# Optimization experiments

Measured on AMD Instinct MI355X. Metric: run time of the kernel, lower is better.

Reference implementation:

```python
import jax, jax.numpy as jnp
import numpy as np

VOL_SHAPE = (192, 192, 192)
BATCH = 2
CHANNELS = 1


def setup_inputs() -> dict:
    key = jax.random.key(0)
    k1, k2 = jax.random.split(key)
    vol = jax.random.normal(k1, (BATCH,) + VOL_SHAPE + (CHANNELS,), dtype=jnp.float32)
    # near-identity affine (3,4) per batch element, as in rigid/affine motion correction
    eye = jnp.concatenate([jnp.eye(3, dtype=jnp.float32), jnp.zeros((3, 1), jnp.float32)], axis=1)
    affine = eye[None] + 0.02 * jax.random.normal(k2, (BATCH, 3, 4), dtype=jnp.float32)
    return {"vol": vol, "affine": affine}


def _warp(vol, affine):
    # vol: [B, D, H, W, C], affine: [B, 3, 4]
    B, D, H, W, C = vol.shape
    shape = (D, H, W)
    # --- affine_to_dense_shift (shift_center=True, ij indexing) ---
    ranges = [jnp.arange(s, dtype=jnp.float32) for s in shape]
    mesh = jnp.stack(jnp.meshgrid(*ranges, indexing='ij'), axis=-1)  # [D,H,W,3]
    center = jnp.array([(s - 1) / 2.0 for s in shape], dtype=jnp.float32)
    centered = mesh - center                                          # shifted grid
    homog = jnp.concatenate([centered, jnp.ones(shape + (1,), jnp.float32)], axis=-1)  # [D,H,W,4]
    loc_aff = jnp.einsum('bij,dhwj->bdhwi', affine, homog)            # [B,D,H,W,3]
    shift = loc_aff - centered                                        # dense warp field
    # --- SpatialTransformer: sample at grid + shift ---
    loc = mesh + shift                                                # [B,D,H,W,3]

    maxl = jnp.array([s - 1 for s in shape], dtype=jnp.float32)

    def interp_one(v, l):
        # v: [D,H,W,C], l: [D,H,W,3]; trilinear interp, clamp-to-edge (fill_value=None)
        cl = jnp.clip(l, 0.0, maxl)
        l0 = jnp.clip(jnp.floor(l), 0.0, maxl)
        l1 = jnp.clip(l0 + 1.0, 0.0, maxl)
        w_c0 = l1 - cl          # weight used with the floor corner (diff_loc1)
        w_c1 = 1.0 - w_c0       # weight used with the ceil corner  (diff_loc0)
        i0 = l0.astype(jnp.int32)
        i1 = l1.astype(jnp.int32)
        out = jnp.zeros(v.shape[:-1] + (v.shape[-1],), v.dtype)
        for c in range(8):  # 2^3 cube corners (fixed small loop)
            bits = ((c >> 2) & 1, (c >> 1) & 1, c & 1)
            idx = [(i1 if b else i0)[..., d] for d, b in enumerate(bits)]
            w = jnp.ones(l.shape[:-1], v.dtype)
            for d, b in enumerate(bits):
                w = w * (w_c1 if b else w_c0)[..., d]
            out = out + v[idx[0], idx[1], idx[2]] * w[..., None]
        return out

    return jax.vmap(interp_one)(vol, loc)


def reference(vol, affine):
    return _warp(vol, affine)
```

## Files before the change

### kernel.cpp

```cpp
#include <hip/hip_runtime.h>

#define DIM 192
#define NB 2

__global__ __launch_bounds__(DIM) void
SpatialTransformer_warp_kernel(const float* __restrict__ vol,
                               const float* __restrict__ affine,
                               float* __restrict__ out) {
    const int w = threadIdx.x;
    const int h = blockIdx.x;
    const int d = blockIdx.y;
    const int b = blockIdx.z;

    const float* __restrict__ A = affine + b * 12;
    const float a00 = A[0], a01 = A[1], a02 = A[2],  a03 = A[3];
    const float a10 = A[4], a11 = A[5], a12 = A[6],  a13 = A[7];
    const float a20 = A[8], a21 = A[9], a22 = A[10], a23 = A[11];

    const float center = (DIM - 1) * 0.5f;
    const float maxl   = (float)(DIM - 1);

    const float cd = (float)d - center;
    const float ch = (float)h - center;
    const float cw = (float)w - center;

    const float ld = a00 * cd + a01 * ch + a02 * cw + a03 + center;
    const float lh = a10 * cd + a11 * ch + a12 * cw + a13 + center;
    const float lw = a20 * cd + a21 * ch + a22 * cw + a23 + center;

    float cl, l0f, l1f;

    cl  = fminf(fmaxf(ld, 0.0f), maxl);
    l0f = fminf(fmaxf(floorf(ld), 0.0f), maxl);
    l1f = fminf(l0f + 1.0f, maxl);
    const float w0d = l1f - cl, w1d = 1.0f - w0d;
    const int i0d = (int)l0f, i1d = (int)l1f;

    cl  = fminf(fmaxf(lh, 0.0f), maxl);
    l0f = fminf(fmaxf(floorf(lh), 0.0f), maxl);
    l1f = fminf(l0f + 1.0f, maxl);
    const float w0h = l1f - cl, w1h = 1.0f - w0h;
    const int i0h = (int)l0f, i1h = (int)l1f;

    cl  = fminf(fmaxf(lw, 0.0f), maxl);
    l0f = fminf(fmaxf(floorf(lw), 0.0f), maxl);
    l1f = fminf(l0f + 1.0f, maxl);
    const float w0w = l1f - cl, w1w = 1.0f - w0w;
    const int i0w = (int)l0f, i1w = (int)l1f;

    const size_t plane = (size_t)DIM * DIM;
    const float* __restrict__ vb = vol + (size_t)b * DIM * plane;

    const float* r00 = vb + (size_t)i0d * plane + (size_t)i0h * DIM;
    const float* r01 = vb + (size_t)i0d * plane + (size_t)i1h * DIM;
    const float* r10 = vb + (size_t)i1d * plane + (size_t)i0h * DIM;
    const float* r11 = vb + (size_t)i1d * plane + (size_t)i1h * DIM;

    const float v000 = r00[i0w], v001 = r00[i1w];
    const float v010 = r01[i0w], v011 = r01[i1w];
    const float v100 = r10[i0w], v101 = r10[i1w];
    const float v110 = r11[i0w], v111 = r11[i1w];

    const float x00 = v000 * w0w + v001 * w1w;
    const float x01 = v010 * w0w + v011 * w1w;
    const float x10 = v100 * w0w + v101 * w1w;
    const float x11 = v110 * w0w + v111 * w1w;

    const float y0 = x00 * w0h + x01 * w1h;
    const float y1 = x10 * w0h + x11 * w1h;

    const float res = y0 * w0d + y1 * w1d;

    out[((size_t)b * DIM + d) * plane + (size_t)h * DIM + w] = res;
}

extern "C" void kernel_launch(void* const* d_in, const int* in_sizes, int n_in,
                              void* d_out, int out_size, void* d_ws, size_t ws_size,
                              hipStream_t stream) {
    const float* vol    = (const float*)d_in[0];
    const float* affine = (const float*)d_in[1];
    float* out = (float*)d_out;

    dim3 grid(DIM, DIM, NB);
    dim3 block(DIM);
    SpatialTransformer_warp_kernel<<<grid, block, 0, stream>>>(vol, affine, out);
}
```

Before: 131.7 us.

## Stage affine-mapped source bounding box in LDS per 3D output tile

Reorganizes the grid into 32x8x8 output tiles with 256-thread blocks. Each block computes the bounding box of its tile's source coordinates and copies that sub-volume into shared memory, then performs the 8-tap trilinear gathers from LDS. A global-memory fallback handles tiles whose footprint exceeds the LDS buffer. It also reformulates the floor/clamp logic with fmed3 and uses nontemporal stores. This aims to replace scattered global gathers with LDS reuse, at the cost of a serial staging loop and a sync.

```diff
diff --git a/kernel.cpp b/kernel.cpp
--- a/kernel.cpp
+++ b/kernel.cpp
@@ -1,16 +1,35 @@
 #include <hip/hip_runtime.h>
 
-#define DIM 192
-#define NB 2
+#define DIM   192
+#define PLANE (DIM * DIM)
+#define NB    2
 
-__global__ __launch_bounds__(DIM) void
+#define TW 32
+#define TH 8
+#define TD 8
+#define SD 14
+#define SH 14
+#define SW 44
+#define LDS_FLOATS (SD * SH * SW)
+
+__device__ __forceinline__ float med3(float x, float lo, float hi) {
+    return __builtin_amdgcn_fmed3f(x, lo, hi);
+}
+
+__global__ __launch_bounds__(256) void
 SpatialTransformer_warp_kernel(const float* __restrict__ vol,
                                const float* __restrict__ affine,
                                float* __restrict__ out) {
-    const int w = threadIdx.x;
-    const int h = blockIdx.x;
-    const int d = blockIdx.y;
-    const int b = blockIdx.z;
+    __shared__ float lds[LDS_FLOATS];
+
+    const int tid = threadIdx.x;
+    const int w   = tid & 31;
+    const int h   = tid >> 5;
+    const int w0  = blockIdx.x * TW;
+    const int h0  = blockIdx.y * TH;
+    const int zt  = blockIdx.z;
+    const int b   = (zt >= DIM / TD) ? 1 : 0;
+    const int d0  = (zt - b * (DIM / TD)) * TD;
 
     const float* __restrict__ A = affine + b * 12;
     const float a00 = A[0], a01 = A[1], a02 = A[2],  a03 = A[3];
@@ -19,59 +38,134 @@
 
     const float center = (DIM - 1) * 0.5f;
     const float maxl   = (float)(DIM - 1);
+    const float maxi0  = (float)(DIM - 2);
 
-    const float cd = (float)d - center;
-    const float ch = (float)h - center;
-    const float cw = (float)w - center;
+    float lmn0, lmx0, lmn1, lmx1, lmn2, lmx2;
+    {
+        float m0, m1, m2;
+#pragma unroll
+        for (int c = 0; c < 8; ++c) {
+            const float fd = (float)(d0 + (((c >> 2) & 1) ? TD - 1 : 0)) - center;
+            const float fh = (float)(h0 + (((c >> 1) & 1) ? TH - 1 : 0)) - center;
+            const float fw = (float)(w0 + ((c & 1) ? TW - 1 : 0)) - center;
+            m0 = a00 * fd + a01 * fh + a02 * fw + a03 + center;
+            m1 = a10 * fd + a11 * fh + a12 * fw + a13 + center;
+            m2 = a20 * fd + a21 * fh + a22 * fw + a23 + center;
+            if (c == 0) {
+                lmn0 = lmx0 = m0; lmn1 = lmx1 = m1; lmn2 = lmx2 = m2;
+            } else {
+                lmn0 = fminf(lmn0, m0); lmx0 = fmaxf(lmx0, m0);
+                lmn1 = fminf(lmn1, m1); lmx1 = fmaxf(lmx1, m1);
+                lmn2 = fminf(lmn2, m2); lmx2 = fmaxf(lmx2, m2);
+            }
+        }
+    }
+    const float flo_d = fminf(floorf(med3(lmn0, 0.0f, maxl)), maxi0);
+    const float flo_h = fminf(floorf(med3(lmn1, 0.0f, maxl)), maxi0);
+    const float flo_w = fminf(floorf(med3(lmn2, 0.0f, maxl)), maxi0);
+    const int lo_d = (int)flo_d, lo_h = (int)flo_h, lo_w = (int)flo_w;
+    const int hi_d = (int)fminf(floorf(med3(lmx0, 0.0f, maxl)), maxi0) + 1;
+    const int hi_h = (int)fminf(floorf(med3(lmx1, 0.0f, maxl)), maxi0) + 1;
+    const int hi_w = (int)fminf(floorf(med3(lmx2, 0.0f, maxl)), maxi0) + 1;
+    const int dd = hi_d - lo_d + 1;
+    const int dh = hi_h - lo_h + 1;
+    const int dw = hi_w - lo_w + 1;
 
-    const float ld = a00 * cd + a01 * ch + a02 * cw + a03 + center;
-    const float lh = a10 * cd + a11 * ch + a12 * cw + a13 + center;
-    const float lw = a20 * cd + a21 * ch + a22 * cw + a23 + center;
+    const float ch = (float)(h0 + h) - center;
+    const float cw = (float)(w0 + w) - center;
+    const float K0 = a01 * ch + a02 * cw + a03 + center;
+    const float K1 = a11 * ch + a12 * cw + a13 + center;
+    const float K2 = a21 * ch + a22 * cw + a23 + center;
 
-    float cl, l0f, l1f;
+    const float* __restrict__ vb = vol + (size_t)b * DIM * PLANE;
+    float* __restrict__ ob = out + ((size_t)b * DIM + d0) * PLANE
+                                 + (size_t)(h0 + h) * DIM + (w0 + w);
 
-    cl  = fminf(fmaxf(ld, 0.0f), maxl);
-    l0f = fminf(fmaxf(floorf(ld), 0.0f), maxl);
-    l1f = fminf(l0f + 1.0f, maxl);
-    const float w0d = l1f - cl, w1d = 1.0f - w0d;
-    const int i0d = (int)l0f, i1d = (int)l1f;
+    const bool fits = (dd <= SD) && (dh <= SH) && (dw <= SW);
 
-    cl  = fminf(fmaxf(lh, 0.0f), maxl);
-    l0f = fminf(fmaxf(floorf(lh), 0.0f), maxl);
-    l1f = fminf(l0f + 1.0f, maxl);
-    const float w0h = l1f - cl, w1h = 1.0f - w0h;
-    const int i0h = (int)l0f, i1h = (int)l1f;
+    if (fits) {
+        const int lane = tid & 63, wid = tid >> 6;
+        const int ys = dw, zs = dh * dw;
+        for (int z = 0; z < dd; ++z) {
+            const float* __restrict__ src = vb + (lo_d + z) * PLANE + lo_h * DIM + lo_w;
+            float* __restrict__ dst = lds + z * zs;
+            for (int y = wid; y < dh; y += 4) {
+                if (lane < dw) dst[y * ys + lane] = src[y * DIM + lane];
+            }
+        }
+        __syncthreads();
 
-    cl  = fminf(fmaxf(lw, 0.0f), maxl);
-    l0f = fminf(fmaxf(floorf(lw), 0.0f), maxl);
-    l1f = fminf(l0f + 1.0f, maxl);
-    const float w0w = l1f - cl, w1w = 1.0f - w0w;
-    const int i0w = (int)l0f, i1w = (int)l1f;
+        const float fzs = (float)zs, fys = (float)ys;
+#pragma unroll
+        for (int dz = 0; dz < TD; ++dz) {
+            const float cd = (float)(d0 + dz) - center;
+            const float ld = a00 * cd + K0;
+            const float lh = a10 * cd + K1;
+            const float lw = a20 * cd + K2;
 
-    const size_t plane = (size_t)DIM * DIM;
-    const float* __restrict__ vb = vol + (size_t)b * DIM * plane;
+            const float td = med3(ld, 0.0f, maxl);
+            const float th = med3(lh, 0.0f, maxl);
+            const float tw = med3(lw, 0.0f, maxl);
+            const float fd = fminf(floorf(td), maxi0);
+            const float fh = fminf(floorf(th), maxi0);
+            const float fw = fminf(floorf(tw), maxi0);
+            const float w0d = fd + 1.0f - td;
+            const float w0h = fh + 1.0f - th;
+            const float w0w = fw + 1.0f - tw;
 
-    const float* r00 = vb + (size_t)i0d * plane + (size_t)i0h * DIM;
-    const float* r01 = vb + (size_t)i0d * plane + (size_t)i1h * DIM;
-    const float* r10 = vb + (size_t)i1d * plane + (size_t)i0h * DIM;
-    const float* r11 = vb + (size_t)i1d * plane + (size_t)i1h * DIM;
+            const int idx = (int)__builtin_fmaf(fd - flo_d, fzs,
+                              __builtin_fmaf(fh - flo_h, fys, fw - flo_w));
+            const float* __restrict__ p = lds + idx;
+            const float v000 = p[0],       v001 = p[1];
+            const float v010 = p[ys],      v011 = p[ys + 1];
+            const float v100 = p[zs],      v101 = p[zs + 1];
+            const float v110 = p[zs + ys], v111 = p[zs + ys + 1];
 
-    const float v000 = r00[i0w], v001 = r00[i1w];
-    const float v010 = r01[i0w], v011 = r01[i1w];
-    const float v100 = r10[i0w], v101 = r10[i1w];
-    const float v110 = r11[i0w], v111 = r11[i1w];
+            const float w1w = 1.0f - w0w, w1h = 1.0f - w0h, w1d = 1.0f - w0d;
+            const float x00 = v000 * w0w + v001 * w1w;
+            const float x01 = v010 * w0w + v011 * w1w;
+            const float x10 = v100 * w0w + v101 * w1w;
+            const float x11 = v110 * w0w + v111 * w1w;
+            const float y0 = x00 * w0h + x01 * w1h;
+            const float y1 = x10 * w0h + x11 * w1h;
+            __builtin_nontemporal_store(y0 * w0d + y1 * w1d, ob + dz * PLANE);
+        }
+    } else {
+#pragma unroll
+        for (int dz = 0; dz < TD; ++dz) {
+            const float cd = (float)(d0 + dz) - center;
+            const float ld = a00 * cd + K0;
+            const float lh = a10 * cd + K1;
+            const float lw = a20 * cd + K2;
 
-    const float x00 = v000 * w0w + v001 * w1w;
-    const float x01 = v010 * w0w + v011 * w1w;
-    const float x10 = v100 * w0w + v101 * w1w;
-    const float x11 = v110 * w0w + v111 * w1w;
+            const float td = med3(ld, 0.0f, maxl);
+            const float th = med3(lh, 0.0f, maxl);
+            const float tw = med3(lw, 0.0f, maxl);
+            const float fd = fminf(floorf(td), maxi0);
+            const float fh = fminf(floorf(th), maxi0);
+            const float fw = fminf(floorf(tw), maxi0);
+            const float w0d = fd + 1.0f - td;
+            const float w0h = fh + 1.0f - th;
+            const float w0w = fw + 1.0f - tw;
 
-    const float y0 = x00 * w0h + x01 * w1h;
-    const float y1 = x10 * w0h + x11 * w1h;
+            const int idx = (int)__builtin_fmaf(fd, (float)PLANE,
+                              __builtin_fmaf(fh, (float)DIM, fw));
+            const float* __restrict__ p = vb + idx;
+            const float v000 = p[0],           v001 = p[1];
+            const float v010 = p[DIM],         v011 = p[DIM + 1];
+            const float v100 = p[PLANE],       v101 = p[PLANE + 1];
+            const float v110 = p[PLANE + DIM], v111 = p[PLANE + DIM + 1];
 
-    const float res = y0 * w0d + y1 * w1d;
-
-    out[((size_t)b * DIM + d) * plane + (size_t)h * DIM + w] = res;
+            const float w1w = 1.0f - w0w, w1h = 1.0f - w0h, w1d = 1.0f - w0d;
+            const float x00 = v000 * w0w + v001 * w1w;
+            const float x01 = v010 * w0w + v011 * w1w;
+            const float x10 = v100 * w0w + v101 * w1w;
+            const float x11 = v110 * w0w + v111 * w1w;
+            const float y0 = x00 * w0h + x01 * w1h;
+            const float y1 = x10 * w0h + x11 * w1h;
+            __builtin_nontemporal_store(y0 * w0d + y1 * w1d, ob + dz * PLANE);
+        }
+    }
 }
 
 extern "C" void kernel_launch(void* const* d_in, const int* in_sizes, int n_in,
@@ -81,7 +175,7 @@
     const float* affine = (const float*)d_in[1];
     float* out = (float*)d_out;
 
-    dim3 grid(DIM, DIM, NB);
-    dim3 block(DIM);
+    dim3 grid(DIM / TW, DIM / TH, NB * (DIM / TD));
+    dim3 block(256);
     SpatialTransformer_warp_kernel<<<grid, block, 0, stream>>>(vol, affine, out);
 }
```

Result: slower. 177.7 us (+34.9%).
